# Optimization experiments

Measured on AMD Instinct MI355X. Metric: run time of the kernel, lower is better.

The kernel has to match this reference:

```python
import jax, jax.numpy as jnp
import numpy as np

HIDDEN = 256
B, L = 4, 4096


def setup_inputs() -> dict:
    key = jax.random.key(0)
    k_in, k_q, k_k, k_v, k_len = jax.random.split(key, 5)
    inputs = jax.random.normal(k_in, (B, L, HIDDEN), dtype=jnp.float32)
    # torch.rand -> uniform [0,1)
    W_query = jax.random.uniform(k_q, (HIDDEN, HIDDEN), dtype=jnp.float32)
    W_key = jax.random.uniform(k_k, (HIDDEN, HIDDEN), dtype=jnp.float32)
    W_value = jax.random.uniform(k_v, (HIDDEN, HIDDEN), dtype=jnp.float32)
    lengths = jax.random.randint(k_len, (B,), 1, L + 1, dtype=jnp.int64)
    return {"inputs": inputs, "W_query": W_query, "W_key": W_key,
            "W_value": W_value, "lengths": lengths}


def reference(inputs, W_query, W_key, W_value, lengths):
    # lengths is unused by the original module (no masking applied).
    # QKV projections (batched matmul with shared weight)
    queries = jnp.einsum('blh,hd->bld', inputs, W_query)
    keys = jnp.einsum('blh,hd->bld', inputs, W_key)
    values = jnp.einsum('blh,hd->bld', inputs, W_value)
    # scaled dot-product attention, full [B, L, L] scores as in original
    scale = 1.0 / jnp.sqrt(jnp.asarray(HIDDEN, dtype=inputs.dtype))
    attn_scores = jnp.einsum('bqd,bkd->bqk', queries, keys) * scale
    attentions = jax.nn.softmax(attn_scores, axis=-1)
    weighted = jnp.einsum('bqk,bkd->bqd', attentions, values)
    return weighted
```

## Files before the change

### kernel.cpp

```cpp
#include <hip/hip_runtime.h>


typedef __bf16 bf16x8 __attribute__((ext_vector_type(8)));
typedef _Float16 f16x8 __attribute__((ext_vector_type(8)));
typedef _Float16 f16x4 __attribute__((ext_vector_type(4)));
typedef float floatx4 __attribute__((ext_vector_type(4)));

#define MFMA16B(a, b, c) __builtin_amdgcn_mfma_f32_16x16x32_bf16(a, b, c, 0, 0, 0)
#define MFMA16F(a, b, c) __builtin_amdgcn_mfma_f32_16x16x32_f16(a, b, c, 0, 0, 0)
#define GLOAD_LDS16(g, l)                                                  \
  __builtin_amdgcn_global_load_lds(                                        \
      (const __attribute__((address_space(1))) void *)(g),                 \
      (__attribute__((address_space(3))) void *)(l), 16, 0, 0)

#define HID 256
#define LSEQ 4096
#define NB 4
#define NTOK (NB * LSEQ)
#define PLANE ((size_t)NTOK * HID)
#define NSPLIT 4
#define QSCALE 0.09016844005556021f


__device__ __forceinline__ void split_bf16(float v, __bf16 &h, __bf16 &l) {
  h = (__bf16)v;
  l = (__bf16)(v - (float)h);
}

__global__ __launch_bounds__(256) void wsplit(const float *__restrict__ Wq,
                                              const float *__restrict__ Wk,
                                              const float *__restrict__ Wv,
                                              __bf16 *__restrict__ Wht,
                                              __bf16 *__restrict__ Wlt) {
  __shared__ float tile[32][256];
  const int wsel = blockIdx.x;
  const int hb = blockIdx.y;
  const float *W = (wsel == 0) ? Wq : (wsel == 1) ? Wk : Wv;
  __bf16 *oh = Wht + wsel * HID * HID;
  __bf16 *ol = Wlt + wsel * HID * HID;
  const int t = threadIdx.x;
  #pragma unroll
  for (int p = 0; p < 8; ++p) {
    int r = p * 4 + (t >> 6);
    int c = (t & 63) * 4;
    *(floatx4 *)&tile[r][c] = *(const floatx4 *)&W[(hb * 32 + r) * HID + c];
  }
  __syncthreads();
  #pragma unroll
  for (int q = 0; q < 4; ++q) {
    int n = q * 64 + (t >> 2);
    int hs = (t & 3) * 8;
    bf16x8 hh, ll;
    #pragma unroll
    for (int i = 0; i < 8; ++i) {
      float v = tile[hs + i][n];
      __bf16 h, l;
      split_bf16(v, h, l);
      hh[i] = h; ll[i] = l;
    }
    *(bf16x8 *)&oh[n * HID + hb * 32 + hs] = hh;
    *(bf16x8 *)&ol[n * HID + hb * 32 + hs] = ll;
  }
}

__global__ __launch_bounds__(256, 2) void qkv_proj(const float *__restrict__ X,
                                                   const __bf16 *__restrict__ Wht,
                                                   const __bf16 *__restrict__ Wlt,
                                                   _Float16 *__restrict__ Qf,
                                                   _Float16 *__restrict__ Kf,
                                                   _Float16 *__restrict__ Vf) {
  __shared__ __bf16 WhS[64 * 256];
  __shared__ __bf16 WlS[64 * 256];
  _Float16 *Tf = (_Float16 *)WhS;

  const int mtile = blockIdx.x;
  const int col0 = blockIdx.y * 64;
  const int tid = threadIdx.x;
  const int w4 = tid >> 6;
  const int lane = tid & 63;
  const int quad = lane >> 4;
  const int ln = lane & 15;
  const int arow = mtile * 64 + w4 * 16 + ln;

  bf16x8 ah[8], al[8];
  #pragma unroll
  for (int kc = 0; kc < 8; ++kc) {
    const float *xp = X + (size_t)arow * HID + kc * 32 + quad * 8;
    floatx4 x0 = *(const floatx4 *)xp;
    floatx4 x1 = *(const floatx4 *)(xp + 4);
    #pragma unroll
    for (int j = 0; j < 4; ++j) {
      __bf16 h, l;
      split_bf16(x0[j], h, l); ah[kc][j] = h; al[kc][j] = l;
      split_bf16(x1[j], h, l); ah[kc][4 + j] = h; al[kc][4 + j] = l;
    }
  }

  const int srow = tid >> 2;
  const int sseg = tid & 3;

  bf16x8 pwh[8], pwl[8];
  {
    const size_t wbase = (size_t)(col0 + srow) * HID;
    #pragma unroll
    for (int j = 0; j < 8; ++j) {
      const int chunk = j * 4 + sseg;
      pwh[j] = *(const bf16x8 *)&Wht[wbase + chunk * 8];
      pwl[j] = *(const bf16x8 *)&Wlt[wbase + chunk * 8];
    }
  }

  for (int w = 0; w < 3; ++w) {
    __syncthreads();
    #pragma unroll
    for (int j = 0; j < 8; ++j) {
      const int chunk = j * 4 + sseg;
      const int dst = srow * 256 + ((chunk ^ (srow & 7)) << 3);
      *(bf16x8 *)&WhS[dst] = pwh[j];
      *(bf16x8 *)&WlS[dst] = pwl[j];
    }
    __syncthreads();

    if (w < 2) {
      const size_t wbase = (size_t)(w + 1) * HID * HID + (size_t)(col0 + srow) * HID;
      #pragma unroll
      for (int j = 0; j < 8; ++j) {
        const int chunk = j * 4 + sseg;
        pwh[j] = *(const bf16x8 *)&Wht[wbase + chunk * 8];
        pwl[j] = *(const bf16x8 *)&Wlt[wbase + chunk * 8];
      }
    }

    floatx4 acc[4] = {};
    #pragma unroll
    for (int kc = 0; kc < 8; ++kc) {
      #pragma unroll
      for (int nt = 0; nt < 4; ++nt) {
        const int a = (nt * 16 + ln) * 256 + (((kc * 4 + quad) ^ (ln & 7)) << 3);
        bf16x8 bh = *(const bf16x8 *)&WhS[a];
        bf16x8 bl = *(const bf16x8 *)&WlS[a];
        acc[nt] = MFMA16B(ah[kc], bh, acc[nt]);
        acc[nt] = MFMA16B(ah[kc], bl, acc[nt]);
        acc[nt] = MFMA16B(al[kc], bh, acc[nt]);
      }
    }

    if (w == 0) {
      #pragma unroll
      for (int nt = 0; nt < 4; ++nt) {
        #pragma unroll
        for (int r = 0; r < 4; ++r) {
          const int orow = mtile * 64 + w4 * 16 + quad * 4 + r;
          const int ocol = col0 + nt * 16 + ln;
          Qf[(size_t)orow * HID + ocol] = (_Float16)(acc[nt][r] * QSCALE);
        }
      }
    } else if (w == 1) {
      __syncthreads();
      #pragma unroll
      for (int nt = 0; nt < 4; ++nt) {
        #pragma unroll
        for (int r = 0; r < 4; ++r) {
          const int tok_l = w4 * 16 + quad * 4 + r;
          const int h_l = nt * 16 + ln;
          Tf[tok_l * 72 + h_l] = (_Float16)acc[nt][r];
        }
      }
      __syncthreads();
      #pragma unroll
      for (int i = 0; i < 2; ++i) {
        const int c = i * 256 + tid;
        const int lane_f = c & 63;
        const int ntf = (c >> 6) & 1;
        const int kcL = (c >> 7) & 1;
        const int t2 = (c >> 8) & 1;
        const int qf = lane_f >> 4;
        const int lnf = lane_f & 15;
        const int tok_l = t2 * 32 + ntf * 16 + lnf;
        f16x8 v = *(const f16x8 *)&Tf[tok_l * 72 + kcL * 32 + qf * 8];
        const int T = mtile * 2 + t2;
        const int kc = (col0 >> 5) + kcL;
        *(f16x8 *)&Kf[(size_t)T * 8192 + ((ntf * 8 + kc) * 64 + lane_f) * 8] = v;
      }
    } else {
      __syncthreads();
      #pragma unroll
      for (int nt = 0; nt < 4; ++nt) {
        #pragma unroll
        for (int r = 0; r < 4; ++r) {
          const int tok_l = w4 * 16 + quad * 4 + r;
          const int d_l = nt * 16 + ln;
          Tf[d_l * 72 + tok_l] = (_Float16)acc[nt][r];
        }
      }
      __syncthreads();
      #pragma unroll
      for (int i = 0; i < 2; ++i) {
        const int c = i * 256 + tid;
        const int lane_f = c & 63;
        const int dtL = (c >> 6) & 3;
        const int t2 = (c >> 8) & 1;
        const int qf = lane_f >> 4;
        const int lnf = lane_f & 15;
        const int d_l = dtL * 16 + lnf;
        f16x4 lo = *(const f16x4 *)&Tf[d_l * 72 + t2 * 32 + 4 * qf];
        f16x4 hi = *(const f16x4 *)&Tf[d_l * 72 + t2 * 32 + 16 + 4 * qf];
        f16x8 v;
        v[0] = lo[0]; v[1] = lo[1]; v[2] = lo[2]; v[3] = lo[3];
        v[4] = hi[0]; v[5] = hi[1]; v[6] = hi[2]; v[7] = hi[3];
        const int T = mtile * 2 + t2;
        const int dt = (col0 >> 4) + dtL;
        *(f16x8 *)&Vf[(size_t)(T * 16 + dt) * 512 + lane_f * 8] = v;
      }
    }
  }
}

__global__ __launch_bounds__(256, 2) void attn(const _Float16 *__restrict__ Qf,
                                               const _Float16 *__restrict__ Kf,
                                               const _Float16 *__restrict__ Vf,
                                               _Float16 *__restrict__ Op,
                                               float *__restrict__ Mp,
                                               float *__restrict__ Lp) {
  __shared__ _Float16 KS[2][8192];
  __shared__ _Float16 VS[2][8192];

  const int bx = blockIdx.x;
  const int ks = bx & 3;
  const int qt = bx >> 2;
  const int b = qt >> 6;
  const int qtl = qt & 63;
  const int tid = threadIdx.x;
  const int w4 = tid >> 6;
  const int lane = tid & 63;
  const int quad = lane >> 4;
  const int ln = lane & 15;
  const int T0 = b * 128 + ks * 32;

  const int qtok = b * LSEQ + qtl * 64 + w4 * 16 + ln;
  f16x8 q[8];
  #pragma unroll
  for (int kc = 0; kc < 8; ++kc)
    q[kc] = *(const f16x8 *)&Qf[(size_t)qtok * HID + kc * 32 + quad * 8];

  const _Float16 *kuni = Kf + (size_t)T0 * 8192;
  const _Float16 *vuni = Vf + (size_t)T0 * 8192;
  const int koff = tid * 8;
  const int voff = lane * 8;

  #pragma unroll
  for (int i = 0; i < 4; ++i)
    GLOAD_LDS16(kuni + i * 2048 + koff, &KS[0][i * 2048 + koff]);
  #pragma unroll
  for (int i = 0; i < 4; ++i)
    GLOAD_LDS16(vuni + i * 2048 + koff, &VS[0][i * 2048 + koff]);

  float m = -1e30f;
  float l = 0.f;
  floatx4 o[16] = {};

  for (int t = 0; t < 32; ++t) {
    const int buf = t & 1;
    asm volatile("s_waitcnt vmcnt(0)" ::: "memory");
    __builtin_amdgcn_s_barrier();
    __builtin_amdgcn_sched_barrier(0);
    if (t < 31) {
      const _Float16 *ksrc = kuni + (size_t)(t + 1) * 8192 + koff;
      const _Float16 *vsrc = vuni + (size_t)(t + 1) * 8192 + koff;
      #pragma unroll
      for (int i = 0; i < 4; ++i)
        GLOAD_LDS16(ksrc + i * 2048, &KS[buf ^ 1][i * 2048 + koff]);
      #pragma unroll
      for (int i = 0; i < 4; ++i)
        GLOAD_LDS16(vsrc + i * 2048, &VS[buf ^ 1][i * 2048 + koff]);
    }
    const _Float16 *Kb = KS[buf];
    const _Float16 *Vb = VS[buf];

    floatx4 s0, s1;
    {
      floatx4 pa0 = {}, pb0 = {}, pa1 = {}, pb1 = {};
      __builtin_amdgcn_s_setprio(1);
      #pragma unroll
      for (int kc = 0; kc < 4; ++kc) {
        pa0 = MFMA16F(*(const f16x8 *)(Kb + kc * 512 + voff), q[kc], pa0);
        pb0 = MFMA16F(*(const f16x8 *)(Kb + (4 + kc) * 512 + voff), q[4 + kc], pb0);
        pa1 = MFMA16F(*(const f16x8 *)(Kb + (8 + kc) * 512 + voff), q[kc], pa1);
        pb1 = MFMA16F(*(const f16x8 *)(Kb + (12 + kc) * 512 + voff), q[4 + kc], pb1);
      }
      __builtin_amdgcn_s_setprio(0);
      s0 = pa0 + pb0;
      s1 = pa1 + pb1;
    }

    float tmax = fmaxf(fmaxf(fmaxf(s0[0], s0[1]), fmaxf(s0[2], s0[3])),
                       fmaxf(fmaxf(s1[0], s1[1]), fmaxf(s1[2], s1[3])));
    tmax = fmaxf(tmax, __shfl_xor(tmax, 16));
    tmax = fmaxf(tmax, __shfl_xor(tmax, 32));
    const float mn = fmaxf(m, tmax);
    const float al = exp2f(m - mn);
    #pragma unroll
    for (int i = 0; i < 4; ++i) {
      s0[i] = exp2f(s0[i] - mn);
      s1[i] = exp2f(s1[i] - mn);
    }
    float rs = ((s0[0] + s0[1]) + (s0[2] + s0[3])) +
               ((s1[0] + s1[1]) + (s1[2] + s1[3]));
    rs += __shfl_xor(rs, 16);
    rs += __shfl_xor(rs, 32);
    l = l * al + rs;
    m = mn;

    f16x8 pf;
    pf[0] = (_Float16)s0[0]; pf[1] = (_Float16)s0[1];
    pf[2] = (_Float16)s0[2]; pf[3] = (_Float16)s0[3];
    pf[4] = (_Float16)s1[0]; pf[5] = (_Float16)s1[1];
    pf[6] = (_Float16)s1[2]; pf[7] = (_Float16)s1[3];

    if (__any(al < 1.0f)) {
      #pragma unroll
      for (int dt = 0; dt < 16; ++dt) {
        o[dt][0] *= al; o[dt][1] *= al; o[dt][2] *= al; o[dt][3] *= al;
      }
    }

    __builtin_amdgcn_s_setprio(1);
    #pragma unroll
    for (int dt = 0; dt < 16; ++dt)
      o[dt] = MFMA16F(*(const f16x8 *)(Vb + dt * 512 + voff), pf, o[dt]);
    __builtin_amdgcn_s_setprio(0);
    __builtin_amdgcn_sched_barrier(0);
  }

  #pragma unroll
  for (int dt = 0; dt < 16; ++dt) {
    f16x4 v4;
    v4[0] = (_Float16)o[dt][0]; v4[1] = (_Float16)o[dt][1];
    v4[2] = (_Float16)o[dt][2]; v4[3] = (_Float16)o[dt][3];
    *(f16x4 *)&Op[(size_t)ks * PLANE + (size_t)qtok * HID + dt * 16 + quad * 4] = v4;
  }
  if (quad == 0) {
    Mp[ks * NTOK + qtok] = m;
    Lp[ks * NTOK + qtok] = l;
  }
}

__global__ __launch_bounds__(256) void merge(const _Float16 *__restrict__ Op,
                                             const float *__restrict__ Mp,
                                             const float *__restrict__ Lp,
                                             float *__restrict__ Out) {
  const int row = blockIdx.x * 4 + (threadIdx.x >> 6);
  const int c = (threadIdx.x & 63) * 4;
  float ms[NSPLIT], ls[NSPLIT];
  #pragma unroll
  for (int s = 0; s < NSPLIT; ++s) {
    ms[s] = Mp[s * NTOK + row];
    ls[s] = Lp[s * NTOK + row];
  }
  const float M = fmaxf(fmaxf(ms[0], ms[1]), fmaxf(ms[2], ms[3]));
  float e[NSPLIT], den = 0.f;
  #pragma unroll
  for (int s = 0; s < NSPLIT; ++s) {
    e[s] = exp2f(ms[s] - M);
    den += ls[s] * e[s];
  }
  const float inv = 1.0f / den;
  floatx4 out = {};
  #pragma unroll
  for (int s = 0; s < NSPLIT; ++s) {
    const f16x4 a = *(const f16x4 *)&Op[(size_t)s * PLANE + (size_t)row * HID + c];
    const float w = e[s] * inv;
    #pragma unroll
    for (int i = 0; i < 4; ++i) out[i] += w * (float)a[i];
  }
  *(floatx4 *)&Out[(size_t)row * HID + c] = out;
}

extern "C" void kernel_launch(void *const *d_in, const int *in_sizes, int n_in,
                              void *d_out, int out_size, void *d_ws, size_t ws_size,
                              hipStream_t stream) {
  const float *X = (const float *)d_in[0];
  const float *Wq = (const float *)d_in[1];
  const float *Wk = (const float *)d_in[2];
  const float *Wv = (const float *)d_in[3];

  _Float16 *ws = (_Float16 *)d_ws;
  _Float16 *Qf = ws;
  _Float16 *Kf = Qf + PLANE;
  _Float16 *Vf = Kf + PLANE;
  __bf16 *Wht = (__bf16 *)(Vf + PLANE);
  __bf16 *Wlt = Wht + 3 * HID * HID;
  _Float16 *Op = (_Float16 *)(Wlt + 3 * HID * HID);
  float *Mp = (float *)(Op + NSPLIT * PLANE);
  float *Lp = Mp + NSPLIT * NTOK;

  wsplit<<<dim3(3, 8), 256, 0, stream>>>(Wq, Wk, Wv, Wht, Wlt);
  qkv_proj<<<dim3(256, 4), 256, 0, stream>>>(X, Wht, Wlt, Qf, Kf, Vf);
  attn<<<NTOK / 64 * NSPLIT, 256, 0, stream>>>(Qf, Kf, Vf, Op, Mp, Lp);
  merge<<<NTOK / 4, 256, 0, stream>>>(Op, Mp, Lp, (float *)d_out);
}
```

Baseline: 222.4 us.

## Process two query tiles per block to reuse K/V loads

Each attention block now handles 128 query rows (two 16-row sub-tiles per wave) instead of 64, reusing every K and V fragment read from LDS for two MFMAs. This halves global K/V traffic and LDS reads per query and halves the grid size. In exchange it doubles the accumulator and Q register footprint (o0/o1, q0/q1), which risks spills or lower occupancy under launch_bounds(256,2), and leaves fewer blocks (1024) to spread across CUs.

```diff
diff --git a/kernel.cpp b/kernel.cpp
--- a/kernel.cpp
+++ b/kernel.cpp
@@ -228,8 +228,8 @@
   const int bx = blockIdx.x;
   const int ks = bx & 3;
   const int qt = bx >> 2;
-  const int b = qt >> 6;
-  const int qtl = qt & 63;
+  const int b = qt >> 5;
+  const int qtl = qt & 31;
   const int tid = threadIdx.x;
   const int w4 = tid >> 6;
   const int lane = tid & 63;
@@ -237,11 +237,14 @@
   const int ln = lane & 15;
   const int T0 = b * 128 + ks * 32;
 
-  const int qtok = b * LSEQ + qtl * 64 + w4 * 16 + ln;
-  f16x8 q[8];
-  #pragma unroll
-  for (int kc = 0; kc < 8; ++kc)
-    q[kc] = *(const f16x8 *)&Qf[(size_t)qtok * HID + kc * 32 + quad * 8];
+  const int qtok0 = b * LSEQ + qtl * 128 + w4 * 16 + ln;
+  const int qtok1 = qtok0 + 64;
+  f16x8 q0[8], q1[8];
+  #pragma unroll
+  for (int kc = 0; kc < 8; ++kc) {
+    q0[kc] = *(const f16x8 *)&Qf[(size_t)qtok0 * HID + kc * 32 + quad * 8];
+    q1[kc] = *(const f16x8 *)&Qf[(size_t)qtok1 * HID + kc * 32 + quad * 8];
+  }
 
   const _Float16 *kuni = Kf + (size_t)T0 * 8192;
   const _Float16 *vuni = Vf + (size_t)T0 * 8192;
@@ -255,9 +258,9 @@
   for (int i = 0; i < 4; ++i)
     GLOAD_LDS16(vuni + i * 2048 + koff, &VS[0][i * 2048 + koff]);
 
-  float m = -1e30f;
-  float l = 0.f;
-  floatx4 o[16] = {};
+  float m0 = -1e30f, m1 = -1e30f;
+  float l0 = 0.f, l1 = 0.f;
+  floatx4 o0[16] = {}, o1[16] = {};
 
   for (int t = 0; t < 32; ++t) {
     const int buf = t & 1;
@@ -277,57 +280,101 @@
     const _Float16 *Kb = KS[buf];
     const _Float16 *Vb = VS[buf];
 
-    floatx4 s0, s1;
+    floatx4 s00, s01, s10, s11;
     {
-      floatx4 pa0 = {}, pb0 = {}, pa1 = {}, pb1 = {};
+      floatx4 a00 = {}, b00 = {}, a01 = {}, b01 = {};
+      floatx4 a10 = {}, b10 = {}, a11 = {}, b11 = {};
       __builtin_amdgcn_s_setprio(1);
       #pragma unroll
       for (int kc = 0; kc < 4; ++kc) {
-        pa0 = MFMA16F(*(const f16x8 *)(Kb + kc * 512 + voff), q[kc], pa0);
-        pb0 = MFMA16F(*(const f16x8 *)(Kb + (4 + kc) * 512 + voff), q[4 + kc], pb0);
-        pa1 = MFMA16F(*(const f16x8 *)(Kb + (8 + kc) * 512 + voff), q[kc], pa1);
-        pb1 = MFMA16F(*(const f16x8 *)(Kb + (12 + kc) * 512 + voff), q[4 + kc], pb1);
+        const f16x8 k0 = *(const f16x8 *)(Kb + kc * 512 + voff);
+        const f16x8 k1 = *(const f16x8 *)(Kb + (4 + kc) * 512 + voff);
+        const f16x8 k2 = *(const f16x8 *)(Kb + (8 + kc) * 512 + voff);
+        const f16x8 k3 = *(const f16x8 *)(Kb + (12 + kc) * 512 + voff);
+        a00 = MFMA16F(k0, q0[kc], a00);
+        a10 = MFMA16F(k0, q1[kc], a10);
+        b00 = MFMA16F(k1, q0[4 + kc], b00);
+        b10 = MFMA16F(k1, q1[4 + kc], b10);
+        a01 = MFMA16F(k2, q0[kc], a01);
+        a11 = MFMA16F(k2, q1[kc], a11);
+        b01 = MFMA16F(k3, q0[4 + kc], b01);
+        b11 = MFMA16F(k3, q1[4 + kc], b11);
       }
       __builtin_amdgcn_s_setprio(0);
-      s0 = pa0 + pb0;
-      s1 = pa1 + pb1;
-    }
-
-    float tmax = fmaxf(fmaxf(fmaxf(s0[0], s0[1]), fmaxf(s0[2], s0[3])),
-                       fmaxf(fmaxf(s1[0], s1[1]), fmaxf(s1[2], s1[3])));
-    tmax = fmaxf(tmax, __shfl_xor(tmax, 16));
-    tmax = fmaxf(tmax, __shfl_xor(tmax, 32));
-    const float mn = fmaxf(m, tmax);
-    const float al = exp2f(m - mn);
-    #pragma unroll
-    for (int i = 0; i < 4; ++i) {
-      s0[i] = exp2f(s0[i] - mn);
-      s1[i] = exp2f(s1[i] - mn);
-    }
-    float rs = ((s0[0] + s0[1]) + (s0[2] + s0[3])) +
-               ((s1[0] + s1[1]) + (s1[2] + s1[3]));
-    rs += __shfl_xor(rs, 16);
-    rs += __shfl_xor(rs, 32);
-    l = l * al + rs;
-    m = mn;
-
-    f16x8 pf;
-    pf[0] = (_Float16)s0[0]; pf[1] = (_Float16)s0[1];
-    pf[2] = (_Float16)s0[2]; pf[3] = (_Float16)s0[3];
-    pf[4] = (_Float16)s1[0]; pf[5] = (_Float16)s1[1];
-    pf[6] = (_Float16)s1[2]; pf[7] = (_Float16)s1[3];
-
-    if (__any(al < 1.0f)) {
+      s00 = a00 + b00; s01 = a01 + b01;
+      s10 = a10 + b10; s11 = a11 + b11;
+    }
+
+    float al0, al1;
+    {
+      float tmax = fmaxf(fmaxf(fmaxf(s00[0], s00[1]), fmaxf(s00[2], s00[3])),
+                         fmaxf(fmaxf(s01[0], s01[1]), fmaxf(s01[2], s01[3])));
+      tmax = fmaxf(tmax, __shfl_xor(tmax, 16));
+      tmax = fmaxf(tmax, __shfl_xor(tmax, 32));
+      const float mn = fmaxf(m0, tmax);
+      al0 = exp2f(m0 - mn);
+      #pragma unroll
+      for (int i = 0; i < 4; ++i) {
+        s00[i] = exp2f(s00[i] - mn);
+        s01[i] = exp2f(s01[i] - mn);
+      }
+      float rs = ((s00[0] + s00[1]) + (s00[2] + s00[3])) +
+                 ((s01[0] + s01[1]) + (s01[2] + s01[3]));
+      rs += __shfl_xor(rs, 16);
+      rs += __shfl_xor(rs, 32);
+      l0 = l0 * al0 + rs;
+      m0 = mn;
+    }
+    {
+      float tmax = fmaxf(fmaxf(fmaxf(s10[0], s10[1]), fmaxf(s10[2], s10[3])),
+                         fmaxf(fmaxf(s11[0], s11[1]), fmaxf(s11[2], s11[3])));
+      tmax = fmaxf(tmax, __shfl_xor(tmax, 16));
+      tmax = fmaxf(tmax, __shfl_xor(tmax, 32));
+      const float mn = fmaxf(m1, tmax);
+      al1 = exp2f(m1 - mn);
+      #pragma unroll
+      for (int i = 0; i < 4; ++i) {
+        s10[i] = exp2f(s10[i] - mn);
+        s11[i] = exp2f(s11[i] - mn);
+      }
+      float rs = ((s10[0] + s10[1]) + (s10[2] + s10[3])) +
+                 ((s11[0] + s11[1]) + (s11[2] + s11[3]));
+      rs += __shfl_xor(rs, 16);
+      rs += __shfl_xor(rs, 32);
+      l1 = l1 * al1 + rs;
+      m1 = mn;
+    }
+
+    f16x8 pf0, pf1;
+    pf0[0] = (_Float16)s00[0]; pf0[1] = (_Float16)s00[1];
+    pf0[2] = (_Float16)s00[2]; pf0[3] = (_Float16)s00[3];
+    pf0[4] = (_Float16)s01[0]; pf0[5] = (_Float16)s01[1];
+    pf0[6] = (_Float16)s01[2]; pf0[7] = (_Float16)s01[3];
+    pf1[0] = (_Float16)s10[0]; pf1[1] = (_Float16)s10[1];
+    pf1[2] = (_Float16)s10[2]; pf1[3] = (_Float16)s10[3];
+    pf1[4] = (_Float16)s11[0]; pf1[5] = (_Float16)s11[1];
+    pf1[6] = (_Float16)s11[2]; pf1[7] = (_Float16)s11[3];
+
+    if (__any(al0 < 1.0f)) {
       #pragma unroll
       for (int dt = 0; dt < 16; ++dt) {
-        o[dt][0] *= al; o[dt][1] *= al; o[dt][2] *= al; o[dt][3] *= al;
+        o0[dt][0] *= al0; o0[dt][1] *= al0; o0[dt][2] *= al0; o0[dt][3] *= al0;
+      }
+    }
+    if (__any(al1 < 1.0f)) {
+      #pragma unroll
+      for (int dt = 0; dt < 16; ++dt) {
+        o1[dt][0] *= al1; o1[dt][1] *= al1; o1[dt][2] *= al1; o1[dt][3] *= al1;
       }
     }
 
     __builtin_amdgcn_s_setprio(1);
     #pragma unroll
-    for (int dt = 0; dt < 16; ++dt)
-      o[dt] = MFMA16F(*(const f16x8 *)(Vb + dt * 512 + voff), pf, o[dt]);
+    for (int dt = 0; dt < 16; ++dt) {
+      const f16x8 vf = *(const f16x8 *)(Vb + dt * 512 + voff);
+      o0[dt] = MFMA16F(vf, pf0, o0[dt]);
+      o1[dt] = MFMA16F(vf, pf1, o1[dt]);
+    }
     __builtin_amdgcn_s_setprio(0);
     __builtin_amdgcn_sched_barrier(0);
   }
@@ -335,13 +382,19 @@
   #pragma unroll
   for (int dt = 0; dt < 16; ++dt) {
     f16x4 v4;
-    v4[0] = (_Float16)o[dt][0]; v4[1] = (_Float16)o[dt][1];
-    v4[2] = (_Float16)o[dt][2]; v4[3] = (_Float16)o[dt][3];
-    *(f16x4 *)&Op[(size_t)ks * PLANE + (size_t)qtok * HID + dt * 16 + quad * 4] = v4;
+    v4[0] = (_Float16)o0[dt][0]; v4[1] = (_Float16)o0[dt][1];
+    v4[2] = (_Float16)o0[dt][2]; v4[3] = (_Float16)o0[dt][3];
+    *(f16x4 *)&Op[(size_t)ks * PLANE + (size_t)qtok0 * HID + dt * 16 + quad * 4] = v4;
+    f16x4 w4v;
+    w4v[0] = (_Float16)o1[dt][0]; w4v[1] = (_Float16)o1[dt][1];
+    w4v[2] = (_Float16)o1[dt][2]; w4v[3] = (_Float16)o1[dt][3];
+    *(f16x4 *)&Op[(size_t)ks * PLANE + (size_t)qtok1 * HID + dt * 16 + quad * 4] = w4v;
   }
   if (quad == 0) {
-    Mp[ks * NTOK + qtok] = m;
-    Lp[ks * NTOK + qtok] = l;
+    Mp[ks * NTOK + qtok0] = m0;
+    Lp[ks * NTOK + qtok0] = l0;
+    Mp[ks * NTOK + qtok1] = m1;
+    Lp[ks * NTOK + qtok1] = l1;
   }
 }
 
@@ -396,6 +449,6 @@
 
   wsplit<<<dim3(3, 8), 256, 0, stream>>>(Wq, Wk, Wv, Wht, Wlt);
   qkv_proj<<<dim3(256, 4), 256, 0, stream>>>(X, Wht, Wlt, Qf, Kf, Vf);
-  attn<<<NTOK / 64 * NSPLIT, 256, 0, stream>>>(Qf, Kf, Vf, Op, Mp, Lp);
+  attn<<<NTOK / 128 * NSPLIT, 256, 0, stream>>>(Qf, Kf, Vf, Op, Mp, Lp);
   merge<<<NTOK / 4, 256, 0, stream>>>(Op, Mp, Lp, (float *)d_out);
 }
```

Result: faster. 209.9 us (-5.6%).
